# Optimization experiments

Measured on AMD Instinct MI355X. Metric: run time of the kernel, lower is better.

Reference implementation:

```python
import jax, jax.numpy as jnp
import numpy as np

ALPHA = 0.1
BETA = float(np.log(0.5 / 4 + 1.0))  # theta=0.5, layer=4


def setup_inputs() -> dict:
    key = jax.random.key(0)
    k = jax.random.split(key, 6)
    B, C, N, K = 1, 128, 40000, 16
    x = jax.random.normal(k[0], (B, C, N, 1), dtype=jnp.float32)
    x_0 = jax.random.normal(k[1], (B, N, C), dtype=jnp.float32)
    edge_index = jax.random.randint(k[2], (2, B, N, K), 0, N)
    W1 = jax.random.normal(k[3], (C, C), dtype=jnp.float32) * 0.05
    W2 = jax.random.normal(k[4], (C, C), dtype=jnp.float32) * 0.05
    bias = jax.random.uniform(k[5], (1, 1, C), dtype=jnp.float32)
    return {"x": x, "x_0": x_0, "edge_index": edge_index, "W1": W1, "W2": W2, "bias": bias}


def reference(x, x_0, edge_index, W1, W2, bias):
    # x: [B, C, N, 1]; x_0: [B, N, C]; edge_index: [2, B, N, K]
    B, C, N, _ = x.shape
    idx = edge_index[0]  # neighbor indices [B, N, K]
    self_idx = jnp.broadcast_to(jnp.arange(N, dtype=idx.dtype)[None, :, None], (B, N, 1))
    idx = jnp.concatenate([idx, self_idx], axis=-1)  # add self loops -> [B, N, K+1]
    deg = idx.shape[-1]  # constant degree K+1
    x2 = x[..., 0]  # [B, C, N]
    # irregular gather of neighbor features: [B, C, N, K+1]
    x_j = jax.vmap(lambda xb, ib: xb[:, ib])(x2, idx)
    aggr = x_j.sum(axis=-1) * (1.0 / deg)  # [B, C, N]
    aggr = jnp.swapaxes(aggr, 1, 2)  # [B, N, C]
    out = (aggr * ((1.0 - ALPHA) * (1.0 - BETA))
           + jnp.einsum('bnc,oc->bno', aggr, W1) * BETA
           + x_0 * (ALPHA * (1.0 - BETA))
           + jnp.einsum('bnc,oc->bno', x_0, W2) * BETA
           + bias)
    out = jax.nn.relu(out)
    return jnp.swapaxes(out, 1, 2)[..., None]  # [B, C, N, 1]
```

## Files before the change

kernel.cpp:

```cpp
#include <hip/hip_runtime.h>

#define N_NODES 40000
#define C_DIM   128
#define K_NBR   16

static constexpr float BETA_F  = 0.11778303565638346f;
static constexpr float C1_F    = 0.7939952679092549f;
static constexpr float C2_F    = 0.08822169643436166f;
static constexpr float INV_DEG = 1.0f / 17.0f;

typedef __attribute__((ext_vector_type(8))) short bf16x8;
typedef __attribute__((ext_vector_type(4))) float f32x4;

__device__ __forceinline__ unsigned pack_bf16x2(float a, float b) {
    unsigned ua = __float_as_uint(a), ub = __float_as_uint(b);
    ua += 0x7fffu + ((ua >> 16) & 1u);
    ub += 0x7fffu + ((ub >> 16) & 1u);
    return (ua >> 16) | (ub & 0xffff0000u);
}
__device__ __forceinline__ float bflo(unsigned u) { return __uint_as_float(u << 16); }
__device__ __forceinline__ float bfhi(unsigned u) { return __uint_as_float(u & 0xffff0000u); }

__global__ __launch_bounds__(256) void prep_kernel(
        const float* __restrict__ x,
        const float* __restrict__ W1,
        const float* __restrict__ W2,
        unsigned* __restrict__ xTb,
        unsigned short* __restrict__ WB) {
    __shared__ unsigned lds[32 * 65];

    const int b = blockIdx.x;
    const int tid = threadIdx.x;

    if (b < 128) {
        const int i = b * 256 + tid;
        const int frag = i >> 9, within = i & 511;
        const int lane = within >> 3, j = within & 7;
        const int otile = frag >> 3, kblk = frag & 7;
        const int o = otile * 16 + (lane & 15);
        const int c = kblk * 32 + ((lane >> 4) << 3) + j;
        float v;
        if (c < 128) {
            v = (BETA_F * W1[o * 128 + c] + (c == o ? C1_F : 0.0f)) * INV_DEG;
        } else {
            const int c2 = c - 128;
            v = BETA_F * W2[o * 128 + c2] + (c2 == o ? C2_F : 0.0f);
        }
        unsigned u = __float_as_uint(v);
        u += 0x7fffu + ((u >> 16) & 1u);
        WB[i] = (unsigned short)(u >> 16);
        return;
    }

    const int nb = (b - 128) * 32;

    const int c2 = tid >> 2;
    const int h  = tid & 3;
    const float* r0 = &x[(size_t)(2 * c2)     * N_NODES + nb + h * 8];
    const float* r1 = &x[(size_t)(2 * c2 + 1) * N_NODES + nb + h * 8];
    const float4 a0 = *(const float4*)(r0);
    const float4 a1 = *(const float4*)(r0 + 4);
    const float4 b0 = *(const float4*)(r1);
    const float4 b1 = *(const float4*)(r1 + 4);

    unsigned* lrow = &lds[h * 8 * 65 + c2];
    lrow[0 * 65] = pack_bf16x2(a0.x, b0.x);
    lrow[1 * 65] = pack_bf16x2(a0.y, b0.y);
    lrow[2 * 65] = pack_bf16x2(a0.z, b0.z);
    lrow[3 * 65] = pack_bf16x2(a0.w, b0.w);
    lrow[4 * 65] = pack_bf16x2(a1.x, b1.x);
    lrow[5 * 65] = pack_bf16x2(a1.y, b1.y);
    lrow[6 * 65] = pack_bf16x2(a1.z, b1.z);
    lrow[7 * 65] = pack_bf16x2(a1.w, b1.w);
    __syncthreads();

    const int n = tid >> 3, q = tid & 7;
    const unsigned* src = &lds[n * 65 + q * 8];
    unsigned* dst = &xTb[(size_t)(nb + n) * 64 + q * 8];
    *(uint4*)&dst[0] = make_uint4(src[0], src[1], src[2], src[3]);
    *(uint4*)&dst[4] = make_uint4(src[4], src[5], src[6], src[7]);
}

__global__ __launch_bounds__(256) void fused4_kernel(
        const unsigned* __restrict__ xTb,
        const float*    __restrict__ x0,
        const int*      __restrict__ e0,
        const bf16x8*   __restrict__ WB,
        const float*    __restrict__ bias,
        float*          __restrict__ out) {
    __shared__ unsigned y[32][132];
    __shared__ int eis[512];

    const int nb   = blockIdx.x * 32;
    const int tid  = threadIdx.x;
    const int lane = tid & 63;
    const int wid  = tid >> 6;

    eis[tid]       = e0[(size_t)nb * K_NBR + tid];
    eis[256 + tid] = e0[(size_t)nb * K_NBR + 256 + tid];
    __syncthreads();

    const int node = tid >> 3;
    const int g8   = tid & 7;
    {
        const float* r = &x0[(size_t)(nb + node) * C_DIM + g8 * 16];
        const float4 v0 = *(const float4*)(r);
        const float4 v1 = *(const float4*)(r + 4);
        const float4 v2 = *(const float4*)(r + 8);
        const float4 v3 = *(const float4*)(r + 12);
        uint4 ua, ub;
        ua.x = pack_bf16x2(v0.x, v0.y);  ua.y = pack_bf16x2(v0.z, v0.w);
        ua.z = pack_bf16x2(v1.x, v1.y);  ua.w = pack_bf16x2(v1.z, v1.w);
        ub.x = pack_bf16x2(v2.x, v2.y);  ub.y = pack_bf16x2(v2.z, v2.w);
        ub.z = pack_bf16x2(v3.x, v3.y);  ub.w = pack_bf16x2(v3.z, v3.w);
        *(uint4*)&y[node][64 + g8 * 8]     = ua;
        *(uint4*)&y[node][64 + g8 * 8 + 4] = ub;
    }

    int jreg[K_NBR];
#pragma unroll
    for (int k = 0; k < K_NBR; ++k) jreg[k] = eis[node * K_NBR + k];

#pragma unroll 1
    for (int q = 0; q < 4; ++q) {
        const int off = q * 16 + 2 * g8;
        const uint2 sv = *(const uint2*)&xTb[(size_t)(nb + node) * 64 + off];
        float s0 = bflo(sv.x), s1 = bfhi(sv.x);
        float s2 = bflo(sv.y), s3 = bfhi(sv.y);
#pragma unroll
        for (int k = 0; k < K_NBR; ++k) {
            const uint2 v = *(const uint2*)&xTb[(size_t)jreg[k] * 64 + off];
            s0 += bflo(v.x); s1 += bfhi(v.x);
            s2 += bflo(v.y); s3 += bfhi(v.y);
        }
        *(uint2*)&y[node][off] =
            make_uint2(pack_bf16x2(s0, s1), pack_bf16x2(s2, s3));
    }
    __syncthreads();

    const int nh = wid & 1;
    const int oh = wid >> 1;
    const int arow = nh * 16 + (lane & 15);
    const int acol = (lane >> 4) * 4;

    bf16x8 afrag[8];
#pragma unroll
    for (int kb = 0; kb < 8; ++kb)
        afrag[kb] = *(const bf16x8*)&y[arow][kb * 16 + acol];

    f32x4 acc[4];
#pragma unroll
    for (int t = 0; t < 4; ++t) {
        f32x4 a = {0.f, 0.f, 0.f, 0.f};
#pragma unroll
        for (int kb = 0; kb < 8; ++kb) {
            bf16x8 bv = WB[((oh * 4 + t) * 8 + kb) * 64 + lane];
            a = __builtin_amdgcn_mfma_f32_16x16x32_bf16(afrag[kb], bv, a, 0, 0, 0);
        }
        acc[t] = a;
    }

    const int rbase = nh * 16 + (lane >> 4) * 4;
#pragma unroll
    for (int t = 0; t < 4; ++t) {
        const int o = oh * 64 + t * 16 + (lane & 15);
        const float bo = bias[o];
        float4 res;
        res.x = fmaxf(acc[t][0] + bo, 0.0f);
        res.y = fmaxf(acc[t][1] + bo, 0.0f);
        res.z = fmaxf(acc[t][2] + bo, 0.0f);
        res.w = fmaxf(acc[t][3] + bo, 0.0f);
        *(float4*)&out[(size_t)o * N_NODES + nb + rbase] = res;
    }
}

extern "C" void kernel_launch(void* const* d_in, const int* in_sizes, int n_in,
                              void* d_out, int out_size, void* d_ws, size_t ws_size,
                              hipStream_t stream) {
    const float* x    = (const float*)d_in[0];
    const float* x0   = (const float*)d_in[1];
    const int*   ei   = (const int*)  d_in[2];
    const float* W1   = (const float*)d_in[3];
    const float* W2   = (const float*)d_in[4];
    const float* bias = (const float*)d_in[5];
    float* out = (float*)d_out;

    unsigned short* WB  = (unsigned short*)d_ws;
    unsigned*       xTb = (unsigned*)((char*)d_ws + 65536);

    hipLaunchKernelGGL(prep_kernel, dim3(1378), dim3(256), 0, stream,
                       x, W1, W2, xTb, WB);
    hipLaunchKernelGGL(fused4_kernel, dim3(1250), dim3(256), 0, stream,
                       xTb, x0, ei, (const bf16x8*)WB, bias, out);
}
```

Measured before the change: 40.63 us.

## Halve node tile to 16 and swizzle block-to-tile mapping for output locality

The fused gather+MFMA kernel now processes 16 nodes per block instead of 32, doubling the grid to 2500 blocks. Each thread gathers 4 channel pairs over 2 passes instead of 4, and each wave computes 2 output tiles instead of 4. A block-index remap interleaves tiles within groups of 16 so adjacent blocks write nearby output columns. The aim is more parallelism and shorter per-thread gather chains to hide latency, at the cost of 16-byte output stores per row and more block overhead.

```diff
diff --git a/kernel.cpp b/kernel.cpp
--- a/kernel.cpp
+++ b/kernel.cpp
@@ -81,40 +81,43 @@
     *(uint4*)&dst[4] = make_uint4(src[4], src[5], src[6], src[7]);
 }
 
-__global__ __launch_bounds__(256) void fused4_kernel(
+__global__ __launch_bounds__(256) void fused7_kernel(
         const unsigned* __restrict__ xTb,
         const float*    __restrict__ x0,
         const int*      __restrict__ e0,
         const bf16x8*   __restrict__ WB,
         const float*    __restrict__ bias,
         float*          __restrict__ out) {
-    __shared__ unsigned y[32][132];
-    __shared__ int eis[512];
+    __shared__ unsigned y[16][132];
+    __shared__ int eis[256];
 
-    const int nb   = blockIdx.x * 32;
-    const int tid  = threadIdx.x;
+    const int b = blockIdx.x;
+    int tile;
+    if (b >= 2496) {
+        tile = b;
+    } else {
+        const int g = b >> 4, w = b & 15;
+        tile = g * 16 + (w & 7) * 2 + (w >> 3);
+    }
+    const int nb  = tile * 16;
+    const int tid = threadIdx.x;
     const int lane = tid & 63;
     const int wid  = tid >> 6;
 
-    eis[tid]       = e0[(size_t)nb * K_NBR + tid];
-    eis[256 + tid] = e0[(size_t)nb * K_NBR + 256 + tid];
+    eis[tid] = e0[(size_t)nb * K_NBR + tid];
     __syncthreads();
 
-    const int node = tid >> 3;
-    const int g8   = tid & 7;
+    const int node = tid >> 4;
+    const int g16  = tid & 15;
+
     {
-        const float* r = &x0[(size_t)(nb + node) * C_DIM + g8 * 16];
+        const float* r = &x0[(size_t)(nb + node) * C_DIM + g16 * 8];
         const float4 v0 = *(const float4*)(r);
         const float4 v1 = *(const float4*)(r + 4);
-        const float4 v2 = *(const float4*)(r + 8);
-        const float4 v3 = *(const float4*)(r + 12);
-        uint4 ua, ub;
+        uint4 ua;
         ua.x = pack_bf16x2(v0.x, v0.y);  ua.y = pack_bf16x2(v0.z, v0.w);
         ua.z = pack_bf16x2(v1.x, v1.y);  ua.w = pack_bf16x2(v1.z, v1.w);
-        ub.x = pack_bf16x2(v2.x, v2.y);  ub.y = pack_bf16x2(v2.z, v2.w);
-        ub.z = pack_bf16x2(v3.x, v3.y);  ub.w = pack_bf16x2(v3.z, v3.w);
-        *(uint4*)&y[node][64 + g8 * 8]     = ua;
-        *(uint4*)&y[node][64 + g8 * 8 + 4] = ub;
+        *(uint4*)&y[node][64 + g16 * 4] = ua;
     }
 
     int jreg[K_NBR];
@@ -122,8 +125,8 @@
     for (int k = 0; k < K_NBR; ++k) jreg[k] = eis[node * K_NBR + k];
 
 #pragma unroll 1
-    for (int q = 0; q < 4; ++q) {
-        const int off = q * 16 + 2 * g8;
+    for (int q = 0; q < 2; ++q) {
+        const int off = q * 32 + 2 * g16;
         const uint2 sv = *(const uint2*)&xTb[(size_t)(nb + node) * 64 + off];
         float s0 = bflo(sv.x), s1 = bfhi(sv.x);
         float s2 = bflo(sv.y), s3 = bfhi(sv.y);
@@ -138,9 +141,7 @@
     }
     __syncthreads();
 
-    const int nh = wid & 1;
-    const int oh = wid >> 1;
-    const int arow = nh * 16 + (lane & 15);
+    const int arow = lane & 15;
     const int acol = (lane >> 4) * 4;
 
     bf16x8 afrag[8];
@@ -148,22 +149,23 @@
     for (int kb = 0; kb < 8; ++kb)
         afrag[kb] = *(const bf16x8*)&y[arow][kb * 16 + acol];
 
-    f32x4 acc[4];
+    f32x4 acc[2];
 #pragma unroll
-    for (int t = 0; t < 4; ++t) {
+    for (int t = 0; t < 2; ++t) {
         f32x4 a = {0.f, 0.f, 0.f, 0.f};
+        const int otile = wid * 2 + t;
 #pragma unroll
         for (int kb = 0; kb < 8; ++kb) {
-            bf16x8 bv = WB[((oh * 4 + t) * 8 + kb) * 64 + lane];
+            bf16x8 bv = WB[(otile * 8 + kb) * 64 + lane];
             a = __builtin_amdgcn_mfma_f32_16x16x32_bf16(afrag[kb], bv, a, 0, 0, 0);
         }
         acc[t] = a;
     }
 
-    const int rbase = nh * 16 + (lane >> 4) * 4;
+    const int rbase = (lane >> 4) * 4;
 #pragma unroll
-    for (int t = 0; t < 4; ++t) {
-        const int o = oh * 64 + t * 16 + (lane & 15);
+    for (int t = 0; t < 2; ++t) {
+        const int o = wid * 32 + t * 16 + (lane & 15);
         const float bo = bias[o];
         float4 res;
         res.x = fmaxf(acc[t][0] + bo, 0.0f);
@@ -190,6 +192,6 @@
 
     hipLaunchKernelGGL(prep_kernel, dim3(1378), dim3(256), 0, stream,
                        x, W1, W2, xTb, WB);
-    hipLaunchKernelGGL(fused4_kernel, dim3(1250), dim3(256), 0, stream,
+    hipLaunchKernelGGL(fused7_kernel, dim3(2500), dim3(256), 0, stream,
                        xTb, x0, ei, (const bf16x8*)WB, bias, out);
 }
```

After: 42.19 us. 1.04x slower.
